# Performance work log

Measured on AMD Instinct MI355X. Metric: run time of the kernel, lower is better.

## Reference

```python
import jax, jax.numpy as jnp
import numpy as np

N = 100000   # nodes
E = 3200000  # edges (avg degree 32)
D = 512      # dim_latent
NEG_SLOPE = 0.01  # nn.LeakyReLU default


def setup_inputs() -> dict:
    key = jax.random.key(0)
    ks = jax.random.split(key, 14)
    weight = jax.random.normal(ks[0], (N,), dtype=jnp.float32)
    significance = jax.random.randint(ks[1], (N,), 0, 2, dtype=jnp.int32)
    src = jax.random.randint(ks[2], (E,), 0, N, dtype=jnp.int32)
    dst = jax.random.randint(ks[3], (E,), 0, N, dtype=jnp.int32)
    emb_table = jax.random.normal(ks[4], (2, 2), dtype=jnp.float32)
    lin_W = jax.random.normal(ks[5], (3, D), dtype=jnp.float32) / np.sqrt(3.0)
    lin_b = jnp.zeros((D,), dtype=jnp.float32)
    s = 1.0 / np.sqrt(D)
    W0 = jax.random.normal(ks[6], (D, D), dtype=jnp.float32) * s
    b0 = jnp.zeros((D,), dtype=jnp.float32)
    W1 = jax.random.normal(ks[7], (D, D), dtype=jnp.float32) * s
    b1 = jnp.zeros((D,), dtype=jnp.float32)
    W2 = jax.random.normal(ks[8], (D, D), dtype=jnp.float32) * s
    b2 = jnp.zeros((D,), dtype=jnp.float32)
    pred_W = jax.random.normal(ks[9], (D, 1), dtype=jnp.float32) * s
    pred_b = jnp.zeros((1,), dtype=jnp.float32)
    return {"weight": weight, "significance": significance, "src": src, "dst": dst,
            "emb_table": emb_table, "lin_W": lin_W, "lin_b": lin_b,
            "W0": W0, "b0": b0, "W1": W1, "b1": b1, "W2": W2, "b2": b2,
            "pred_W": pred_W, "pred_b": pred_b}


def _gcn_layer(feat, src, dst, n_out, n_in, W, b):
    # DGL GraphConv norm='both' with self-loops already folded into degrees.
    h = feat * n_out[:, None]                                   # [N, D] src-normalize
    agg = jax.ops.segment_sum(h[src], dst, num_segments=N)      # SpMM aggregate
    agg = agg + h                                               # self-loop message
    agg = agg * n_in[:, None]                                   # dst-normalize
    return agg @ W + b


def reference(weight, significance, src, dst, emb_table, lin_W, lin_b,
              W0, b0, W1, b1, W2, b2, pred_W, pred_b):
    ones = jnp.ones((E,), dtype=jnp.float32)
    deg_out = jax.ops.segment_sum(ones, src, num_segments=N) + 1.0  # +1 self-loop
    deg_in = jax.ops.segment_sum(ones, dst, num_segments=N) + 1.0
    n_out = jax.lax.rsqrt(deg_out)
    n_in = jax.lax.rsqrt(deg_in)

    sig = emb_table[significance]                            # [N, 2]
    feats = jnp.concatenate([weight[:, None], sig], axis=1)  # [N, 3]
    feats = feats @ lin_W + lin_b                            # [N, D]

    h = _gcn_layer(feats, src, dst, n_out, n_in, W0, b0)
    for W, b in ((W1, b1), (W2, b2)):
        h = jnp.where(h >= 0, h, NEG_SLOPE * h)              # LeakyReLU
        h = _gcn_layer(h, src, dst, n_out, n_in, W, b)

    # NOTE: original forward's `if self.train:` is always truthy (method object),
    # so it always returns the prediction logits.
    logits = h @ pred_W + pred_b                             # [N, 1]
    return logits
```

## Files before the change

### kernel.cpp

```cpp
#include <hip/hip_runtime.h>

#define N_NODES 100000
#define M_PAD 100096
#define N_EDGES 3200000
#define DIM 512
#define SLOTS 80
#define NEG_SLOPE 0.01f

typedef _Float16 f16;
typedef _Float16 f16x8 __attribute__((ext_vector_type(8)));
typedef float f32x4 __attribute__((ext_vector_type(4)));

__device__ __forceinline__ void load_lds16(const void* g, void* l) {
  __builtin_amdgcn_global_load_lds(
      (const __attribute__((address_space(1))) void*)g,
      (__attribute__((address_space(3))) void*)l, 16, 0, 0);
}


__global__ void k_pre(const int* __restrict__ src, const int* __restrict__ dst,
                      int* __restrict__ cnt_o, int* __restrict__ cnt_i,
                      int* __restrict__ ell) {
  int e = blockIdx.x * blockDim.x + threadIdx.x;
  if (e < N_EDGES) {
    int s = src[e];
    atomicAdd(&cnt_o[s], 1);
    int d = dst[e];
    int p = atomicAdd(&cnt_i[d], 1);
    if (p < SLOTS) ell[(size_t)d * SLOTS + p] = s;
  }
}

__global__ void k_norms(const int* __restrict__ cnt_o, const int* __restrict__ cnt_i,
                        float* __restrict__ n_out, float* __restrict__ n_in) {
  int i = blockIdx.x * blockDim.x + threadIdx.x;
  if (i < N_NODES) {
    n_out[i] = rsqrtf((float)cnt_o[i] + 1.0f);
    n_in[i] = rsqrtf((float)cnt_i[i] + 1.0f);
  }
}

__global__ void k_wt(const float* __restrict__ W0, const float* __restrict__ W1,
                     f16* __restrict__ Wt) {
  int idx = blockIdx.x * blockDim.x + threadIdx.x;
  int l = idx >> 18;
  int r = idx & 262143;
  int n = r >> 9, k = r & 511;
  const float* W = (l == 0) ? W0 : W1;
  Wt[idx] = (f16)W[k * DIM + n];
}

__global__ void k_wp(const float* __restrict__ W2, const float* __restrict__ b2,
                     const float* __restrict__ pW, const float* __restrict__ pb,
                     float* __restrict__ wt_vec, float* __restrict__ c_out) {
  int k = blockIdx.x, lane = threadIdx.x;
  if (k < DIM) {
    float s = 0.f;
    for (int n = lane; n < DIM; n += 64) s += W2[k * DIM + n] * pW[n];
#pragma unroll
    for (int off = 32; off; off >>= 1) s += __shfl_down(s, off, 64);
    if (lane == 0) wt_vec[k] = s;
  } else {
    float s = 0.f;
    for (int n = lane; n < DIM; n += 64) s += b2[n] * pW[n];
#pragma unroll
    for (int off = 32; off; off >>= 1) s += __shfl_down(s, off, 64);
    if (lane == 0) c_out[0] = s + pb[0];
  }
}


__global__ void k_feats(const float* __restrict__ weight, const int* __restrict__ sig,
                        const float* __restrict__ emb, const float* __restrict__ linW,
                        const float* __restrict__ linb, const float* __restrict__ n_out,
                        f16* __restrict__ Xs) {
  int wid = threadIdx.x >> 6, lane = threadIdx.x & 63;
  int node = blockIdx.x * 4 + wid;
  float w = weight[node];
  int sg = sig[node];
  float s0 = emb[sg * 2], s1 = emb[sg * 2 + 1];
  float no = n_out[node];
  int d0 = lane * 8;
  f16x8 v;
#pragma unroll
  for (int k = 0; k < 8; k++) {
    int d = d0 + k;
    float f = (w * linW[d] + s0 * linW[DIM + d] + s1 * linW[2 * DIM + d] + linb[d]) * no;
    v[k] = (f16)f;
  }
  *(f16x8*)(Xs + (size_t)node * DIM + d0) = v;
}

__global__ void k_spmm(const f16* __restrict__ Xs, f16* __restrict__ A,
                       const int* __restrict__ ell, const int* __restrict__ cnt_i,
                       const float* __restrict__ n_in) {
  int wid = threadIdx.x >> 6, lane = threadIdx.x & 63;
  int node = blockIdx.x * 4 + wid;
  int d0 = lane * 8;
  float acc[8];
  {
    f16x8 v = *(const f16x8*)(Xs + (size_t)node * DIM + d0);
#pragma unroll
    for (int k = 0; k < 8; k++) acc[k] = (float)v[k];
  }
  int deg = cnt_i[node];
  if (deg > SLOTS) deg = SLOTS;
  const int* erow = ell + (size_t)node * SLOTS;
  const f16* base = Xs + d0;
  int j = 0;
  for (; j + 8 <= deg; j += 8) {
    int ix[8];
#pragma unroll
    for (int u = 0; u < 8; u++) ix[u] = erow[j + u];
    f16x8 v[8];
#pragma unroll
    for (int u = 0; u < 8; u++) v[u] = *(const f16x8*)(base + (size_t)ix[u] * DIM);
#pragma unroll
    for (int u = 0; u < 8; u++)
#pragma unroll
      for (int k = 0; k < 8; k++) acc[k] += (float)v[u][k];
  }
  for (; j < deg; ++j) {
    int sn = erow[j];
    f16x8 v = *(const f16x8*)(base + (size_t)sn * DIM);
#pragma unroll
    for (int k = 0; k < 8; k++) acc[k] += (float)v[k];
  }
  float ni = n_in[node];
  f16x8 o;
#pragma unroll
  for (int k = 0; k < 8; k++) o[k] = (f16)(acc[k] * ni);
  __builtin_nontemporal_store(o, (f16x8*)(A + (size_t)node * DIM + d0));
}

__global__ __launch_bounds__(256) void k_gemm(const f16* __restrict__ A, const f16* __restrict__ Wt,
                                              const float* __restrict__ bias,
                                              const float* __restrict__ n_out,
                                              f16* __restrict__ Y) {
  __shared__ __align__(1024) char smem[32768];
  const int tid = threadIdx.x;
  const int wid = tid >> 6, lane = tid & 63;
  const int lr = lane & 15, lk = lane >> 4;
  const int wr = wid >> 1, wc = wid & 1;
  const int cb = blockIdx.x * 128;
  const int rb = blockIdx.y * 128;
  const int ls = lane >> 3;
  const int ss = lane & 7;

  f32x4 acc[4][4];
#pragma unroll
  for (int i = 0; i < 4; i++)
#pragma unroll
    for (int j = 0; j < 4; j++) acc[i][j] = (f32x4){0.f, 0.f, 0.f, 0.f};

  for (int kb = 0; kb < DIM; kb += 64) {
#pragma unroll
    for (int i = 0; i < 4; i++) {
      int c = wid * 4 + i;
      int r = c * 8 + ls;
      int goff = (ss * 16) ^ ((r & 7) << 4);
      const char* ga = (const char*)A + ((size_t)(rb + r) * DIM + kb) * 2 + goff;
      load_lds16(ga, smem + c * 1024);
      const char* gw = (const char*)Wt + ((size_t)(cb + r) * DIM + kb) * 2 + goff;
      load_lds16(gw, smem + 16384 + c * 1024);
    }
    __syncthreads();
#pragma unroll
    for (int kk = 0; kk < 2; kk++) {
      f16x8 a[4], b[4];
#pragma unroll
      for (int fm = 0; fm < 4; fm++) {
        int row = wr * 64 + fm * 16 + lr;
        int byt = row * 128 + ((kk * 64 + lk * 16) ^ ((row & 7) << 4));
        a[fm] = *(const f16x8*)(smem + byt);
      }
#pragma unroll
      for (int fn = 0; fn < 4; fn++) {
        int row = wc * 64 + fn * 16 + lr;
        int byt = row * 128 + ((kk * 64 + lk * 16) ^ ((row & 7) << 4));
        b[fn] = *(const f16x8*)(smem + 16384 + byt);
      }
#pragma unroll
      for (int fm = 0; fm < 4; fm++)
#pragma unroll
        for (int fn = 0; fn < 4; fn++)
          acc[fm][fn] = __builtin_amdgcn_mfma_f32_16x16x32_f16(a[fm], b[fn], acc[fm][fn], 0, 0, 0);
    }
    __syncthreads();
  }

#pragma unroll
  for (int fn = 0; fn < 4; fn++) {
    int col = cb + wc * 64 + fn * 16 + lr;
    float bv = bias[col];
#pragma unroll
    for (int fm = 0; fm < 4; fm++) {
#pragma unroll
      for (int r = 0; r < 4; r++) {
        int row = rb + wr * 64 + fm * 16 + lk * 4 + r;
        if (row < N_NODES) {
          float v = acc[fm][fn][r] + bv;
          v = (v >= 0.f) ? v : NEG_SLOPE * v;
          v *= n_out[row];
          Y[(size_t)row * DIM + col] = (f16)v;
        }
      }
    }
  }
}

__global__ void k_gemv(const f16* __restrict__ H, const float* __restrict__ wt_vec,
                       float* __restrict__ y) {
  int wid = threadIdx.x >> 6, lane = threadIdx.x & 63;
  int node = blockIdx.x * 4 + wid;
  int d0 = lane * 8;
  f16x8 v = *(const f16x8*)(H + (size_t)node * DIM + d0);
  float s = 0.f;
#pragma unroll
  for (int k = 0; k < 8; k++) s += (float)v[k] * wt_vec[d0 + k];
#pragma unroll
  for (int off = 32; off; off >>= 1) s += __shfl_down(s, off, 64);
  if (lane == 0) y[node] = s;
}

__global__ void k_sagg(const float* __restrict__ y, const int* __restrict__ ell,
                       const int* __restrict__ cnt_i, const float* __restrict__ n_in,
                       const float* __restrict__ c_out, float* __restrict__ out) {
  int i = blockIdx.x * blockDim.x + threadIdx.x;
  if (i >= N_NODES) return;
  int deg = cnt_i[i];
  if (deg > SLOTS) deg = SLOTS;
  const int* erow = ell + (size_t)i * SLOTS;
  float s = y[i];
  int j = 0;
  for (; j + 8 <= deg; j += 8) {
    int4 a = *(const int4*)(erow + j);
    int4 b = *(const int4*)(erow + j + 4);
    s += y[a.x] + y[a.y] + y[a.z] + y[a.w];
    s += y[b.x] + y[b.y] + y[b.z] + y[b.w];
  }
  for (; j < deg; ++j) s += y[erow[j]];
  out[i] = n_in[i] * s + c_out[0];
}

extern "C" void kernel_launch(void* const* d_in, const int* in_sizes, int n_in_cnt,
                              void* d_out, int out_size, void* d_ws, size_t ws_size,
                              hipStream_t stream) {
  const float* weight = (const float*)d_in[0];
  const int* sig = (const int*)d_in[1];
  const int* src = (const int*)d_in[2];
  const int* dst = (const int*)d_in[3];
  const float* emb = (const float*)d_in[4];
  const float* linW = (const float*)d_in[5];
  const float* linb = (const float*)d_in[6];
  const float* W0 = (const float*)d_in[7];
  const float* b0 = (const float*)d_in[8];
  const float* W1 = (const float*)d_in[9];
  const float* b1 = (const float*)d_in[10];
  const float* W2 = (const float*)d_in[11];
  const float* b2 = (const float*)d_in[12];
  const float* pW = (const float*)d_in[13];
  const float* pb = (const float*)d_in[14];
  float* out = (float*)d_out;

  char* ws = (char*)d_ws;
  size_t off = 0;
  auto alloc = [&](size_t bytes) {
    void* p = ws + off;
    off += (bytes + 255) & ~(size_t)255;
    return p;
  };
  int* cnt_o = (int*)alloc((size_t)N_NODES * 4);
  int* cnt_i = (int*)alloc((size_t)N_NODES * 4);
  float* n_out = (float*)alloc((size_t)N_NODES * 4);
  float* n_in = (float*)alloc((size_t)N_NODES * 4);
  int* ell = (int*)alloc((size_t)N_NODES * SLOTS * 4);
  f16* Wt = (f16*)alloc((size_t)2 * DIM * DIM * 2);
  float* wt_vec = (float*)alloc((size_t)DIM * 4);
  float* c_out = (float*)alloc(256);
  float* yv = (float*)alloc((size_t)N_NODES * 4);
  f16* B0 = (f16*)alloc((size_t)M_PAD * DIM * 2);
  f16* B1 = (f16*)alloc((size_t)M_PAD * DIM * 2);

  dim3 blk(256);
  hipMemsetAsync(cnt_o, 0, (char*)n_out - (char*)cnt_o, stream);
  k_pre<<<(N_EDGES + 255) / 256, blk, 0, stream>>>(src, dst, cnt_o, cnt_i, ell);
  k_norms<<<(N_NODES + 255) / 256, blk, 0, stream>>>(cnt_o, cnt_i, n_out, n_in);
  k_wt<<<2 * DIM * DIM / 256, blk, 0, stream>>>(W0, W1, Wt);
  k_wp<<<DIM + 1, 64, 0, stream>>>(W2, b2, pW, pb, wt_vec, c_out);
  k_feats<<<N_NODES / 4, blk, 0, stream>>>(weight, sig, emb, linW, linb, n_out, B0);

  dim3 ggrid(DIM / 128, M_PAD / 128);
  for (int l = 0; l < 2; l++) {
    k_spmm<<<N_NODES / 4, blk, 0, stream>>>(B0, B1, ell, cnt_i, n_in);
    const float* bl = (l == 0) ? b0 : b1;
    k_gemm<<<ggrid, blk, 0, stream>>>(B1, Wt + (size_t)l * DIM * DIM, bl, n_out, B0);
  }
  k_gemv<<<N_NODES / 4, blk, 0, stream>>>(B0, wt_vec, yv);
  k_sagg<<<(N_NODES + 255) / 256, blk, 0, stream>>>(yv, ell, cnt_i, n_in, c_out, out);
}
```

Baseline: 1.644 ms.

## Slab-partition feature layout and degree-sorted node order for SpMM gather

Feature matrices are stored as 32 column slabs of 16 halves per node, so each SpMM block gathers within one slab of about 3.2MB that can stay cache-resident. Nodes are processed in an order sorted by in-degree (histogram, scan, permutation), which balances work across lanes, and each lane pair handles one node's 16-wide slab row. The GEMM loads, GEMM epilogue stores and GEMV are rewritten to match the new layout. In exchange, ELL indices are re-read once per slab (32 times per layer), the GEMM epilogue stores become strided 2-byte writes, and three small preprocessing kernels are added.

```diff
diff --git a/kernel.cpp b/kernel.cpp
--- a/kernel.cpp
+++ b/kernel.cpp
@@ -5,6 +5,8 @@
 #define N_EDGES 3200000
 #define DIM 512
 #define SLOTS 80
+#define NSLAB 32
+#define GRPS 782
 #define NEG_SLOPE 0.01f
 
 typedef _Float16 f16;
@@ -37,6 +39,25 @@
   if (i < N_NODES) {
     n_out[i] = rsqrtf((float)cnt_o[i] + 1.0f);
     n_in[i] = rsqrtf((float)cnt_i[i] + 1.0f);
+  }
+}
+
+__global__ void k_dh(const int* __restrict__ cnt_i, int* __restrict__ bins) {
+  int i = blockIdx.x * blockDim.x + threadIdx.x;
+  if (i < N_NODES) atomicAdd(&bins[min(cnt_i[i], 127)], 1);
+}
+__global__ void k_dscan(const int* __restrict__ bins, int* __restrict__ bins2) {
+  if (threadIdx.x == 0) {
+    int s = 0;
+    for (int i = 0; i < 128; i++) { int v = bins[i]; bins2[i] = s; s += v; }
+  }
+}
+__global__ void k_dperm(const int* __restrict__ cnt_i, int* __restrict__ bins2,
+                        int* __restrict__ perm) {
+  int i = blockIdx.x * blockDim.x + threadIdx.x;
+  if (i < N_NODES) {
+    int pos = atomicAdd(&bins2[min(cnt_i[i], 127)], 1);
+    perm[pos] = i;
   }
 }
 
@@ -88,41 +109,45 @@
     float f = (w * linW[d] + s0 * linW[DIM + d] + s1 * linW[2 * DIM + d] + linb[d]) * no;
     v[k] = (f16)f;
   }
-  *(f16x8*)(Xs + (size_t)node * DIM + d0) = v;
+  *(f16x8*)(Xs + ((size_t)(lane >> 1) * M_PAD + node) * 16 + (lane & 1) * 8) = v;
 }
 
 __global__ void k_spmm(const f16* __restrict__ Xs, f16* __restrict__ A,
                        const int* __restrict__ ell, const int* __restrict__ cnt_i,
-                       const float* __restrict__ n_in) {
-  int wid = threadIdx.x >> 6, lane = threadIdx.x & 63;
-  int node = blockIdx.x * 4 + wid;
-  int d0 = lane * 8;
+                       const float* __restrict__ n_in, const int* __restrict__ perm) {
+  const int wv = threadIdx.x >> 6, lane = threadIdx.x & 63;
+  const int slab = blockIdx.x / GRPS;
+  const int grp = blockIdx.x % GRPS;
+  const int p = lane >> 1, h = lane & 1;
+  const int slot = grp * 128 + wv * 32 + p;
+  if (slot >= N_NODES) return;
+  const int node = perm[slot];
+  const f16* Xsl = Xs + (size_t)slab * M_PAD * 16;
   float acc[8];
   {
-    f16x8 v = *(const f16x8*)(Xs + (size_t)node * DIM + d0);
-#pragma unroll
-    for (int k = 0; k < 8; k++) acc[k] = (float)v[k];
+    f16x8 sv = *(const f16x8*)(Xsl + (size_t)node * 16 + h * 8);
+#pragma unroll
+    for (int k = 0; k < 8; k++) acc[k] = (float)sv[k];
   }
   int deg = cnt_i[node];
   if (deg > SLOTS) deg = SLOTS;
   const int* erow = ell + (size_t)node * SLOTS;
-  const f16* base = Xs + d0;
   int j = 0;
-  for (; j + 8 <= deg; j += 8) {
-    int ix[8];
-#pragma unroll
-    for (int u = 0; u < 8; u++) ix[u] = erow[j + u];
-    f16x8 v[8];
-#pragma unroll
-    for (int u = 0; u < 8; u++) v[u] = *(const f16x8*)(base + (size_t)ix[u] * DIM);
-#pragma unroll
-    for (int u = 0; u < 8; u++)
+  for (; j + 4 <= deg; j += 4) {
+    int ix[4];
+#pragma unroll
+    for (int u = 0; u < 4; u++) ix[u] = __builtin_nontemporal_load(erow + j + u);
+    f16x8 v[4];
+#pragma unroll
+    for (int u = 0; u < 4; u++) v[u] = *(const f16x8*)(Xsl + (size_t)ix[u] * 16 + h * 8);
+#pragma unroll
+    for (int u = 0; u < 4; u++)
 #pragma unroll
       for (int k = 0; k < 8; k++) acc[k] += (float)v[u][k];
   }
   for (; j < deg; ++j) {
-    int sn = erow[j];
-    f16x8 v = *(const f16x8*)(base + (size_t)sn * DIM);
+    int sn = __builtin_nontemporal_load(erow + j);
+    f16x8 v = *(const f16x8*)(Xsl + (size_t)sn * 16 + h * 8);
 #pragma unroll
     for (int k = 0; k < 8; k++) acc[k] += (float)v[k];
   }
@@ -130,7 +155,7 @@
   f16x8 o;
 #pragma unroll
   for (int k = 0; k < 8; k++) o[k] = (f16)(acc[k] * ni);
-  __builtin_nontemporal_store(o, (f16x8*)(A + (size_t)node * DIM + d0));
+  __builtin_nontemporal_store(o, (f16x8*)(A + ((size_t)slab * M_PAD + node) * 16 + h * 8));
 }
 
 __global__ __launch_bounds__(256) void k_gemm(const f16* __restrict__ A, const f16* __restrict__ Wt,
@@ -159,7 +184,9 @@
       int c = wid * 4 + i;
       int r = c * 8 + ls;
       int goff = (ss * 16) ^ ((r & 7) << 4);
-      const char* ga = (const char*)A + ((size_t)(rb + r) * DIM + kb) * 2 + goff;
+      int ch = goff >> 4;
+      const char* ga = (const char*)A +
+          (((size_t)((kb >> 4) + (ch >> 1)) * M_PAD + (rb + r)) * 16 + (ch & 1) * 8) * 2;
       load_lds16(ga, smem + c * 1024);
       const char* gw = (const char*)Wt + ((size_t)(cb + r) * DIM + kb) * 2 + goff;
       load_lds16(gw, smem + 16384 + c * 1024);
@@ -193,6 +220,7 @@
   for (int fn = 0; fn < 4; fn++) {
     int col = cb + wc * 64 + fn * 16 + lr;
     float bv = bias[col];
+    size_t ybase = (size_t)(col >> 4) * M_PAD * 16 + (col & 15);
 #pragma unroll
     for (int fm = 0; fm < 4; fm++) {
 #pragma unroll
@@ -202,7 +230,7 @@
           float v = acc[fm][fn][r] + bv;
           v = (v >= 0.f) ? v : NEG_SLOPE * v;
           v *= n_out[row];
-          Y[(size_t)row * DIM + col] = (f16)v;
+          Y[ybase + (size_t)row * 16] = (f16)v;
         }
       }
     }
@@ -214,7 +242,7 @@
   int wid = threadIdx.x >> 6, lane = threadIdx.x & 63;
   int node = blockIdx.x * 4 + wid;
   int d0 = lane * 8;
-  f16x8 v = *(const f16x8*)(H + (size_t)node * DIM + d0);
+  f16x8 v = *(const f16x8*)(H + ((size_t)(lane >> 1) * M_PAD + node) * 16 + (lane & 1) * 8);
   float s = 0.f;
 #pragma unroll
   for (int k = 0; k < 8; k++) s += (float)v[k] * wt_vec[d0 + k];
@@ -272,8 +300,11 @@
   };
   int* cnt_o = (int*)alloc((size_t)N_NODES * 4);
   int* cnt_i = (int*)alloc((size_t)N_NODES * 4);
+  int* bins = (int*)alloc(512);
+  int* bins2 = (int*)alloc(512);
   float* n_out = (float*)alloc((size_t)N_NODES * 4);
   float* n_in = (float*)alloc((size_t)N_NODES * 4);
+  int* perm = (int*)alloc((size_t)N_NODES * 4);
   int* ell = (int*)alloc((size_t)N_NODES * SLOTS * 4);
   f16* Wt = (f16*)alloc((size_t)2 * DIM * DIM * 2);
   float* wt_vec = (float*)alloc((size_t)DIM * 4);
@@ -283,16 +314,20 @@
   f16* B1 = (f16*)alloc((size_t)M_PAD * DIM * 2);
 
   dim3 blk(256);
-  hipMemsetAsync(cnt_o, 0, (char*)n_out - (char*)cnt_o, stream);
+  hipMemsetAsync(cnt_o, 0, ((char*)bins + 512) - (char*)cnt_o, stream);
   k_pre<<<(N_EDGES + 255) / 256, blk, 0, stream>>>(src, dst, cnt_o, cnt_i, ell);
   k_norms<<<(N_NODES + 255) / 256, blk, 0, stream>>>(cnt_o, cnt_i, n_out, n_in);
+  k_dh<<<(N_NODES + 255) / 256, blk, 0, stream>>>(cnt_i, bins);
+  k_dscan<<<1, 64, 0, stream>>>(bins, bins2);
+  k_dperm<<<(N_NODES + 255) / 256, blk, 0, stream>>>(cnt_i, bins2, perm);
   k_wt<<<2 * DIM * DIM / 256, blk, 0, stream>>>(W0, W1, Wt);
   k_wp<<<DIM + 1, 64, 0, stream>>>(W2, b2, pW, pb, wt_vec, c_out);
   k_feats<<<N_NODES / 4, blk, 0, stream>>>(weight, sig, emb, linW, linb, n_out, B0);
 
+  dim3 sgrid(GRPS * NSLAB);
   dim3 ggrid(DIM / 128, M_PAD / 128);
   for (int l = 0; l < 2; l++) {
-    k_spmm<<<N_NODES / 4, blk, 0, stream>>>(B0, B1, ell, cnt_i, n_in);
+    k_spmm<<<sgrid, blk, 0, stream>>>(B0, B1, ell, cnt_i, n_in, perm);
     const float* bl = (l == 0) ? b0 : b1;
     k_gemm<<<ggrid, blk, 0, stream>>>(B1, Wt + (size_t)l * DIM * DIM, bl, n_out, B0);
   }
```

New measurement: 3.811 ms. 2.32x slower.
